# Optimization experiments

Hardware: AMD Instinct MI355X
Metric: run time of the kernel (lower is better)

Reference implementation:

```python
import jax, jax.numpy as jnp
import numpy as np

B, S, D = 2, 4096, 512
H = 8
W = 512            # local attention window size
HD = D // H        # head dim
NC = S // W        # number of chunks
HALF = W // 2      # symmetric half-window


def setup_inputs() -> dict:
    key = jax.random.key(0)
    ks = jax.random.split(key, 12)
    s = 1.0 / np.sqrt(D)
    return {
        "val": jax.random.normal(ks[0], (B, S, D), jnp.float32),
        "Wq": jax.random.normal(ks[1], (D, D), jnp.float32) * s,
        "bq": jnp.zeros((D,), jnp.float32),
        "Wk": jax.random.normal(ks[2], (D, D), jnp.float32) * s,
        "bk": jnp.zeros((D,), jnp.float32),
        "Wv": jax.random.normal(ks[3], (D, D), jnp.float32) * s,
        "bv": jnp.zeros((D,), jnp.float32),
        "Wo": jax.random.normal(ks[4], (D, D), jnp.float32) * s,
        "bo": jnp.zeros((D,), jnp.float32),
        "gamma": jnp.ones((D,), jnp.float32),
        "beta": jnp.zeros((D,), jnp.float32),
    }


def _heads(x):
    # [B,S,D] -> [B,H,S,HD]
    return x.reshape(B, S, H, HD).transpose(0, 2, 1, 3)


def _gather_neighbors(x):
    # x: [B,H,S,HD] -> [B,H,NC,3W,HD] (prev | cur | next chunk, zero-padded at ends)
    xp = jnp.pad(x, ((0, 0), (0, 0), (W, W), (0, 0)))
    xc = xp.reshape(B, H, NC + 2, W, HD)
    return jnp.concatenate([xc[:, :, :-2], xc[:, :, 1:-1], xc[:, :, 2:]], axis=3)


def _local_attention(x, Wq, bq, Wk, bk, Wv, bv, Wo, bo):
    q = _heads(x @ Wq + bq)
    k = _heads(x @ Wk + bk)
    v = _heads(x @ Wv + bv)

    qc = q.reshape(B, H, NC, W, HD)            # chunked queries
    kn = _gather_neighbors(k)                  # [B,H,NC,3W,HD]
    vn = _gather_neighbors(v)

    scale = 1.0 / np.sqrt(HD)
    scores = jnp.einsum("bhcqd,bhckd->bhcqk", qc, kn) * scale  # [B,H,NC,W,3W]

    # banded mask: key relative position in [-HALF, HALF], and key index in [0,S)
    qi = jnp.arange(W)[:, None]
    kj = jnp.arange(3 * W)[None, :]
    band = jnp.abs(kj - W - qi) <= HALF                          # [W,3W]
    key_pos = (jnp.arange(NC)[:, None, None] - 1) * W + kj[None]  # [NC,1,3W]
    valid = (key_pos >= 0) & (key_pos < S)                       # [NC,1,3W]
    mask = band[None] & valid                                    # [NC,W,3W]

    scores = jnp.where(mask[None, None], scores, jnp.float32(-1e9))
    p = jax.nn.softmax(scores, axis=-1)
    o = jnp.einsum("bhcqk,bhckd->bhcqd", p, vn)                  # [B,H,NC,W,HD]
    o = o.reshape(B, H, S, HD).transpose(0, 2, 1, 3).reshape(B, S, D)
    return o @ Wo + bo


def _layer_norm(x, gamma, beta, eps=1e-5):
    mu = jnp.mean(x, axis=-1, keepdims=True)
    var = jnp.mean(jnp.square(x - mu), axis=-1, keepdims=True)
    return (x - mu) * jax.lax.rsqrt(var + eps) * gamma + beta


def reference(val, Wq, bq, Wk, bk, Wv, bv, Wo, bo, gamma, beta):
    attn_out = _local_attention(val, Wq, bq, Wk, bk, Wv, bv, Wo, bo)
    return _layer_norm(val + attn_out, gamma, beta)
```

## Files before the change

kernel.cpp:

```cpp
#include <hip/hip_runtime.h>
#include <hip/hip_bf16.h>

#define BATCH 2
#define SEQ   4096
#define DIM   512
#define NHEAD 8
#define HDIM  64
#define ROWS  (BATCH*SEQ)

typedef float  fx4   __attribute__((ext_vector_type(4)));
typedef __bf16 bf16x8 __attribute__((ext_vector_type(8)));
typedef unsigned short ushort_t;
typedef unsigned short usx4 __attribute__((ext_vector_type(4)));
typedef unsigned short usx8 __attribute__((ext_vector_type(8)));

static __device__ __forceinline__ float b2f(ushort_t v) {
    union { unsigned int u; float f; } c; c.u = ((unsigned int)v) << 16; return c.f;
}
static __device__ __forceinline__ ushort_t f2b(float f) {
    union { float f; unsigned int u; } c; c.f = f;
    unsigned int u = c.u;
    unsigned int r = (u + 0x7FFFu + ((u >> 16) & 1u)) >> 16;
    return (ushort_t)r;
}
static __device__ __forceinline__ void gload16(const ushort_t* g, ushort_t* l) {
    __builtin_amdgcn_global_load_lds(
        (const __attribute__((address_space(1))) unsigned int*)g,
        (__attribute__((address_space(3))) unsigned int*)l, 16, 0, 0);
}

__global__ __launch_bounds__(256) void cvt_bf16_kernel(const float* __restrict__ x,
                                                       ushort_t* __restrict__ y, int n) {
    int i = (blockIdx.x * 256 + threadIdx.x) * 4;
    if (i < n) {
        fx4 v = *(const fx4*)(x + i);
        usx4 o; o.x = f2b(v.x); o.y = f2b(v.y); o.z = f2b(v.z); o.w = f2b(v.w);
        *(usx4*)(y + i) = o;
    }
}

__global__ __launch_bounds__(256) void transpose4_bf16_kernel(
    const float* __restrict__ W0, const float* __restrict__ W1,
    const float* __restrict__ W2, const float* __restrict__ W3,
    ushort_t* __restrict__ T0, ushort_t* __restrict__ T1,
    ushort_t* __restrict__ T2, ushort_t* __restrict__ T3) {
    const float* W; ushort_t* WT;
    switch (blockIdx.y) {
        case 0: W = W0; WT = T0; break;
        case 1: W = W1; WT = T1; break;
        case 2: W = W2; WT = T2; break;
        default: W = W3; WT = T3; break;
    }
    __shared__ float tile[64][65];
    int r0 = (blockIdx.x & 7) * 64;
    int c0 = (blockIdx.x >> 3) * 64;
    int tid = threadIdx.x;
    for (int idx = tid; idx < 4096; idx += 256) {
        int rr = idx >> 6, cc = idx & 63;
        tile[rr][cc] = W[(c0 + rr) * 512 + (r0 + cc)];
    }
    __syncthreads();
    for (int idx = tid; idx < 4096; idx += 256) {
        int rr = idx >> 6, cc = idx & 63;
        WT[(size_t)(r0 + rr) * 512 + (c0 + cc)] = f2b(tile[cc][rr]);
    }
}

__global__ __launch_bounds__(256) void gemm128_kernel(
    const ushort_t* __restrict__ A,
    const ushort_t* __restrict__ BT0, const ushort_t* __restrict__ BT1, const ushort_t* __restrict__ BT2,
    const float* __restrict__ b0, const float* __restrict__ b1, const float* __restrict__ b2,
    ushort_t* __restrict__ C0, ushort_t* __restrict__ C1, ushort_t* __restrict__ C2) {

    const ushort_t* BT; const float* bias; ushort_t* C;
    if (blockIdx.z == 0)      { BT = BT0; bias = b0; C = C0; }
    else if (blockIdx.z == 1) { BT = BT1; bias = b1; C = C1; }
    else                      { BT = BT2; bias = b2; C = C2; }

    __shared__ ushort_t As[128 * 32];
    __shared__ ushort_t Bs[128 * 32];

    const int tid  = threadIdx.x;
    const int wave = tid >> 6;
    const int lane = tid & 63;
    const int lm   = lane & 15;
    const int quad = lane >> 4;
    const int wm   = wave >> 1;
    const int wn   = wave & 1;

    const int m0t = blockIdx.x * 128;
    const int n0t = blockIdx.y * 128;

    const int srow = tid >> 2, sgc = tid & 3;
    const ushort_t* ga0 = A  + (size_t)(m0t + srow) * 512 + sgc * 8;
    const ushort_t* ga1 = A  + (size_t)(m0t + srow + 64) * 512 + sgc * 8;
    const ushort_t* gb0 = BT + (size_t)(n0t + srow) * 512 + sgc * 8;
    const ushort_t* gb1 = BT + (size_t)(n0t + srow + 64) * 512 + sgc * 8;
    ushort_t* la0 = As + tid * 8;
    ushort_t* la1 = As + (tid + 256) * 8;
    ushort_t* lb0 = Bs + tid * 8;
    ushort_t* lb1 = Bs + (tid + 256) * 8;

    const int aoff = (wm * 64 + lm) * 32 + quad * 8;
    const int boff = (wn * 64 + lm) * 32 + quad * 8;

    fx4 acc[4][4];
    #pragma unroll
    for (int i = 0; i < 4; ++i)
        #pragma unroll
        for (int j = 0; j < 4; ++j) acc[i][j] = 0;

    for (int k0 = 0; k0 < 512; k0 += 32) {
        __syncthreads();
        gload16(ga0 + k0, la0);
        gload16(ga1 + k0, la1);
        gload16(gb0 + k0, lb0);
        gload16(gb1 + k0, lb1);
        __syncthreads();

        bf16x8 af[4], bfr[4];
        #pragma unroll
        for (int ms = 0; ms < 4; ++ms) af[ms]  = *(const bf16x8*)&As[aoff + ms * 512];
        #pragma unroll
        for (int ns = 0; ns < 4; ++ns) bfr[ns] = *(const bf16x8*)&Bs[boff + ns * 512];
        #pragma unroll
        for (int ms = 0; ms < 4; ++ms)
            #pragma unroll
            for (int ns = 0; ns < 4; ++ns)
                acc[ms][ns] = __builtin_amdgcn_mfma_f32_16x16x32_bf16(af[ms], bfr[ns], acc[ms][ns], 0, 0, 0);
    }

    const int crow0 = m0t + wm * 64 + quad * 4;
    const int ccol0 = n0t + wn * 64 + lm;

    if (blockIdx.z == 2) {
        #pragma unroll
        for (int ns = 0; ns < 4; ++ns) {
            int col = ccol0 + ns * 16;
            int h = col >> 6, d = col & 63;
            float bv = bias[col];
            #pragma unroll
            for (int ms = 0; ms < 4; ++ms) {
                int m = crow0 + ms * 16;
                int bb = m >> 12, s0 = m & 4095;
                usx4 o;
                o.x = f2b(acc[ms][ns][0] + bv); o.y = f2b(acc[ms][ns][1] + bv);
                o.z = f2b(acc[ms][ns][2] + bv); o.w = f2b(acc[ms][ns][3] + bv);
                *(usx4*)(C + (((size_t)(bb * 8 + h) * 64 + d) * 4096 + s0)) = o;
            }
        }
    } else {
        #pragma unroll
        for (int ns = 0; ns < 4; ++ns) {
            int col = ccol0 + ns * 16;
            float bv = bias[col];
            #pragma unroll
            for (int ms = 0; ms < 4; ++ms) {
                #pragma unroll
                for (int r = 0; r < 4; ++r) {
                    C[(size_t)(crow0 + ms * 16 + r) * 512 + col] = f2b(acc[ms][ns][r] + bv);
                }
            }
        }
    }
}

__global__ __launch_bounds__(256) void attn_mfma_kernel(
    const ushort_t* __restrict__ Qb, const ushort_t* __restrict__ Kb,
    const ushort_t* __restrict__ Vt, ushort_t* __restrict__ Ob) {

    __shared__ ushort_t Klds[64 * 64];
    __shared__ ushort_t Vlds[64 * 64];
    __shared__ ushort_t Plds[4 * 16 * 64];

    const int tid  = threadIdx.x;
    const int wave = tid >> 6;
    const int lane = tid & 63;
    const int lm   = lane & 15;
    const int quad = lane >> 4;

    const int bh = blockIdx.y;
    const int b = bh >> 3, h = bh & 7;
    const int q0 = blockIdx.x * 64;
    const int qw = q0 + wave * 16;

    const ushort_t* qp = Qb + ((size_t)(b * SEQ + qw + lm)) * 512 + h * 64 + quad * 8;
    bf16x8 qf0 = *(const bf16x8*)qp;
    bf16x8 qf1 = *(const bf16x8*)(qp + 32);

    int koff[2][4], voff[2][4];
    #pragma unroll
    for (int ks = 0; ks < 2; ++ks) {
        #pragma unroll
        for (int tn = 0; tn < 4; ++tn) {
            int key = tn * 16 + lm;
            koff[ks][tn] = key * 64 + (((ks * 4 + quad) ^ (key & 7)) * 8);
            int d = tn * 16 + lm;
            voff[ks][tn] = d * 64 + (((ks * 4 + quad) ^ (d & 7)) * 8);
        }
    }
    int poff[2];
    #pragma unroll
    for (int ks = 0; ks < 2; ++ks)
        poff[ks] = lm * 64 + (((ks * 4 + quad) ^ (lm & 7) ^ ((lm >> 3) << 1)) * 8);
    int pwoff[4][4];
    #pragma unroll
    for (int tn = 0; tn < 4; ++tn) {
        #pragma unroll
        for (int r = 0; r < 4; ++r) {
            int row = quad * 4 + r;
            int col = tn * 16 + lm;
            pwoff[tn][r] = row * 64 + (((col >> 3) ^ (row & 7) ^ ((row >> 3) << 1)) * 8) + (col & 7);
        }
    }
    ushort_t* Pl = Plds + wave * 1024;

    const int skey = tid >> 3;
    const int sdg  = tid & 7;
    const size_t kgbase = ((size_t)b * SEQ) * 512 + h * 64 + sdg * 8;
    const size_t vgbase = ((size_t)bh * 64) * 4096 + sdg * 8;
    const int l0 = skey * 64 + ((sdg ^ (skey & 7)) * 8);
    const int l1 = l0 + 32 * 64;

    fx4 oacc[4];
    oacc[0] = 0; oacc[1] = 0; oacc[2] = 0; oacc[3] = 0;
    float l[4] = {0.f, 0.f, 0.f, 0.f};

    for (int kt = 0; kt < 9; ++kt) {
        int ts = q0 - 256 + kt * 64;
        if (ts < 0 || ts >= SEQ) continue;

        __syncthreads();
        {
            usx8 k0v = *(const usx8*)(Kb + kgbase + (size_t)(ts + skey) * 512);
            usx8 k1v = *(const usx8*)(Kb + kgbase + (size_t)(ts + skey + 32) * 512);
            usx8 v0v = *(const usx8*)(Vt + vgbase + (size_t)skey * 4096 + ts);
            usx8 v1v = *(const usx8*)(Vt + vgbase + (size_t)(skey + 32) * 4096 + ts);
            *(usx8*)&Klds[l0] = k0v;
            *(usx8*)&Klds[l1] = k1v;
            *(usx8*)&Vlds[l0] = v0v;
            *(usx8*)&Vlds[l1] = v1v;
        }
        __syncthreads();

        fx4 sacc[4];
        sacc[0] = 0; sacc[1] = 0; sacc[2] = 0; sacc[3] = 0;
        #pragma unroll
        for (int ks = 0; ks < 2; ++ks) {
            bf16x8 a = ks ? qf1 : qf0;
            #pragma unroll
            for (int tn = 0; tn < 4; ++tn) {
                bf16x8 bk = *(const bf16x8*)&Klds[koff[ks][tn]];
                sacc[tn] = __builtin_amdgcn_mfma_f32_16x16x32_bf16(a, bk, sacc[tn], 0, 0, 0);
            }
        }

        float ps[4] = {0.f, 0.f, 0.f, 0.f};
        #pragma unroll
        for (int tn = 0; tn < 4; ++tn) {
            int kg = ts + tn * 16 + lm;
            #pragma unroll
            for (int r = 0; r < 4; ++r) {
                int qg = qw + quad * 4 + r;
                int dlt = kg - qg;
                float p = (dlt <= 256 && dlt >= -256) ? __expf(sacc[tn][r] * 0.125f) : 0.0f;
                ps[r] += p;
                Pl[pwoff[tn][r]] = f2b(p);
            }
        }
        #pragma unroll
        for (int r = 0; r < 4; ++r) {
            float v = ps[r];
            v += __shfl_xor(v, 1); v += __shfl_xor(v, 2);
            v += __shfl_xor(v, 4); v += __shfl_xor(v, 8);
            l[r] += v;
        }

        #pragma unroll
        for (int ks = 0; ks < 2; ++ks) {
            bf16x8 ap = *(const bf16x8*)&Pl[poff[ks]];
            #pragma unroll
            for (int tn = 0; tn < 4; ++tn) {
                bf16x8 bv = *(const bf16x8*)&Vlds[voff[ks][tn]];
                oacc[tn] = __builtin_amdgcn_mfma_f32_16x16x32_bf16(ap, bv, oacc[tn], 0, 0, 0);
            }
        }
    }

    #pragma unroll
    for (int r = 0; r < 4; ++r) l[r] = 1.0f / l[r];
    ushort_t* ob = Ob + ((size_t)(b * SEQ + qw + quad * 4)) * 512 + h * 64 + lm;
    #pragma unroll
    for (int tn = 0; tn < 4; ++tn) {
        #pragma unroll
        for (int r = 0; r < 4; ++r) {
            ob[(size_t)r * 512 + tn * 16] = f2b(oacc[tn][r] * l[r]);
        }
    }
}

__global__ __launch_bounds__(256) void ln_kernel(
    const float* __restrict__ x, const ushort_t* __restrict__ ob,
    const float* __restrict__ gamma, const float* __restrict__ beta,
    float* __restrict__ out) {

    int row  = blockIdx.x * 4 + (threadIdx.x >> 6);
    int lane = threadIdx.x & 63;

    const float*    xp = x  + (size_t)row * 512 + lane * 8;
    const ushort_t* op = ob + (size_t)row * 512 + lane * 8;

    fx4 xa = ((const fx4*)xp)[0];
    fx4 xb = ((const fx4*)xp)[1];
    usx4 oa = ((const usx4*)op)[0];
    usx4 oc = ((const usx4*)op)[1];
    fx4 va, vb;
    va.x = xa.x + b2f(oa.x); va.y = xa.y + b2f(oa.y); va.z = xa.z + b2f(oa.z); va.w = xa.w + b2f(oa.w);
    vb.x = xb.x + b2f(oc.x); vb.y = xb.y + b2f(oc.y); vb.z = xb.z + b2f(oc.z); vb.w = xb.w + b2f(oc.w);

    float s = va.x + va.y + va.z + va.w + vb.x + vb.y + vb.z + vb.w;
    #pragma unroll
    for (int m = 32; m > 0; m >>= 1) s += __shfl_xor(s, m);
    float mu = s * (1.0f / 512.0f);

    fx4 da = va - mu;
    fx4 db = vb - mu;
    float ss = da.x*da.x + da.y*da.y + da.z*da.z + da.w*da.w
             + db.x*db.x + db.y*db.y + db.z*db.z + db.w*db.w;
    #pragma unroll
    for (int m = 32; m > 0; m >>= 1) ss += __shfl_xor(ss, m);
    float rstd = rsqrtf(ss * (1.0f / 512.0f) + 1e-5f);

    const fx4* gp = (const fx4*)(gamma + lane * 8);
    const fx4* bp = (const fx4*)(beta  + lane * 8);
    fx4 g0 = gp[0], g1 = gp[1], b0 = bp[0], b1 = bp[1];

    float* outp = out + (size_t)row * 512 + lane * 8;
    fx4 r0 = da * rstd * g0 + b0;
    fx4 r1 = db * rstd * g1 + b1;
    ((fx4*)outp)[0] = r0;
    ((fx4*)outp)[1] = r1;
}

extern "C" void kernel_launch(void* const* d_in, const int* in_sizes, int n_in,
                              void* d_out, int out_size, void* d_ws, size_t ws_size,
                              hipStream_t stream) {
    const float* val   = (const float*)d_in[0];
    const float* Wq    = (const float*)d_in[1];
    const float* bq    = (const float*)d_in[2];
    const float* Wk    = (const float*)d_in[3];
    const float* bk    = (const float*)d_in[4];
    const float* Wv    = (const float*)d_in[5];
    const float* bv    = (const float*)d_in[6];
    const float* Wo    = (const float*)d_in[7];
    const float* bo    = (const float*)d_in[8];
    const float* gamma = (const float*)d_in[9];
    const float* beta  = (const float*)d_in[10];
    float* out = (float*)d_out;

    char* w = (char*)d_ws;
    ushort_t* xb    = (ushort_t*)w; w += (size_t)ROWS * 512 * 2;
    ushort_t* WqT   = (ushort_t*)w; w += 512 * 512 * 2;
    ushort_t* WkT   = (ushort_t*)w; w += 512 * 512 * 2;
    ushort_t* WvT   = (ushort_t*)w; w += 512 * 512 * 2;
    ushort_t* WoT   = (ushort_t*)w; w += 512 * 512 * 2;
    ushort_t* Qb    = (ushort_t*)w; w += (size_t)ROWS * 512 * 2;
    ushort_t* Kb    = (ushort_t*)w; w += (size_t)ROWS * 512 * 2;
    ushort_t* Vtb   = (ushort_t*)w; w += (size_t)ROWS * 512 * 2;
    ushort_t* attnb = (ushort_t*)w; w += (size_t)ROWS * 512 * 2;
    ushort_t* obuf  = (ushort_t*)w; w += (size_t)ROWS * 512 * 2;

    int nelem = ROWS * 512;
    cvt_bf16_kernel<<<nelem / (256 * 4), 256, 0, stream>>>(val, xb, nelem);
    transpose4_bf16_kernel<<<dim3(64, 4), 256, 0, stream>>>(
        Wq, Wk, Wv, Wo, WqT, WkT, WvT, WoT);

    gemm128_kernel<<<dim3(ROWS / 128, 4, 3), 256, 0, stream>>>(
        xb, WqT, WkT, WvT, bq, bk, bv, Qb, Kb, Vtb);

    attn_mfma_kernel<<<dim3(SEQ / 64, BATCH * NHEAD), 256, 0, stream>>>(Qb, Kb, Vtb, attnb);

    gemm128_kernel<<<dim3(ROWS / 128, 4, 1), 256, 0, stream>>>(
        attnb, WoT, WoT, WoT, bo, bo, bo, obuf, obuf, obuf);

    ln_kernel<<<ROWS / 4, 256, 0, stream>>>(val, obuf, gamma, beta, out);
}
```

Measured before the change: 169.6 us.

## Enlarge attention query tile, prefetch K/V, skip masked tiles, MFMA row sums

The attention kernel now gives each block 128 queries (32 per wave), so every K/V tile loaded into LDS is reused by twice as many queries. The next K/V tile is prefetched into registers while the current one is computed. Waves skip tiles that lie entirely outside their band, and the mask check runs only on edge tiles. Row sums of P come from an extra MFMA against a ones vector instead of shuffle reductions. The GEMM also stages a 64-wide K slice per barrier pair, halving the number of barriers. In exchange the kernel uses more registers and launches half as many attention blocks, which could reduce occupancy.

```diff
diff --git a/kernel.cpp b/kernel.cpp
--- a/kernel.cpp
+++ b/kernel.cpp
@@ -77,8 +77,8 @@
     else if (blockIdx.z == 1) { BT = BT1; bias = b1; C = C1; }
     else                      { BT = BT2; bias = b2; C = C2; }
 
-    __shared__ ushort_t As[128 * 32];
-    __shared__ ushort_t Bs[128 * 32];
+    __shared__ ushort_t As[2][128 * 32];
+    __shared__ ushort_t Bs[2][128 * 32];
 
     const int tid  = threadIdx.x;
     const int wave = tid >> 6;
@@ -96,10 +96,6 @@
     const ushort_t* ga1 = A  + (size_t)(m0t + srow + 64) * 512 + sgc * 8;
     const ushort_t* gb0 = BT + (size_t)(n0t + srow) * 512 + sgc * 8;
     const ushort_t* gb1 = BT + (size_t)(n0t + srow + 64) * 512 + sgc * 8;
-    ushort_t* la0 = As + tid * 8;
-    ushort_t* la1 = As + (tid + 256) * 8;
-    ushort_t* lb0 = Bs + tid * 8;
-    ushort_t* lb1 = Bs + (tid + 256) * 8;
 
     const int aoff = (wm * 64 + lm) * 32 + quad * 8;
     const int boff = (wn * 64 + lm) * 32 + quad * 8;
@@ -110,24 +106,30 @@
         #pragma unroll
         for (int j = 0; j < 4; ++j) acc[i][j] = 0;
 
-    for (int k0 = 0; k0 < 512; k0 += 32) {
+    for (int k0 = 0; k0 < 512; k0 += 64) {
         __syncthreads();
-        gload16(ga0 + k0, la0);
-        gload16(ga1 + k0, la1);
-        gload16(gb0 + k0, lb0);
-        gload16(gb1 + k0, lb1);
+        #pragma unroll
+        for (int p = 0; p < 2; ++p) {
+            gload16(ga0 + k0 + p * 32, &As[p][tid * 8]);
+            gload16(ga1 + k0 + p * 32, &As[p][(tid + 256) * 8]);
+            gload16(gb0 + k0 + p * 32, &Bs[p][tid * 8]);
+            gload16(gb1 + k0 + p * 32, &Bs[p][(tid + 256) * 8]);
+        }
         __syncthreads();
 
-        bf16x8 af[4], bfr[4];
-        #pragma unroll
-        for (int ms = 0; ms < 4; ++ms) af[ms]  = *(const bf16x8*)&As[aoff + ms * 512];
-        #pragma unroll
-        for (int ns = 0; ns < 4; ++ns) bfr[ns] = *(const bf16x8*)&Bs[boff + ns * 512];
-        #pragma unroll
-        for (int ms = 0; ms < 4; ++ms)
-            #pragma unroll
-            for (int ns = 0; ns < 4; ++ns)
-                acc[ms][ns] = __builtin_amdgcn_mfma_f32_16x16x32_bf16(af[ms], bfr[ns], acc[ms][ns], 0, 0, 0);
+        #pragma unroll
+        for (int p = 0; p < 2; ++p) {
+            bf16x8 af[4], bfr[4];
+            #pragma unroll
+            for (int ms = 0; ms < 4; ++ms) af[ms]  = *(const bf16x8*)&As[p][aoff + ms * 512];
+            #pragma unroll
+            for (int ns = 0; ns < 4; ++ns) bfr[ns] = *(const bf16x8*)&Bs[p][boff + ns * 512];
+            #pragma unroll
+            for (int ms = 0; ms < 4; ++ms)
+                #pragma unroll
+                for (int ns = 0; ns < 4; ++ns)
+                    acc[ms][ns] = __builtin_amdgcn_mfma_f32_16x16x32_bf16(af[ms], bfr[ns], acc[ms][ns], 0, 0, 0);
+        }
     }
 
     const int crow0 = m0t + wm * 64 + quad * 4;
@@ -171,7 +173,7 @@
 
     __shared__ ushort_t Klds[64 * 64];
     __shared__ ushort_t Vlds[64 * 64];
-    __shared__ ushort_t Plds[4 * 16 * 64];
+    __shared__ ushort_t Plds[4 * 32 * 72];
 
     const int tid  = threadIdx.x;
     const int wave = tid >> 6;
@@ -181,12 +183,16 @@
 
     const int bh = blockIdx.y;
     const int b = bh >> 3, h = bh & 7;
-    const int q0 = blockIdx.x * 64;
-    const int qw = q0 + wave * 16;
-
-    const ushort_t* qp = Qb + ((size_t)(b * SEQ + qw + lm)) * 512 + h * 64 + quad * 8;
-    bf16x8 qf0 = *(const bf16x8*)qp;
-    bf16x8 qf1 = *(const bf16x8*)(qp + 32);
+    const int q0 = blockIdx.x * 128;
+    const int qw = q0 + wave * 32;
+
+    bf16x8 qf[2][2];
+    #pragma unroll
+    for (int qs = 0; qs < 2; ++qs) {
+        const ushort_t* qp = Qb + ((size_t)(b * SEQ + qw + qs * 16 + lm)) * 512 + h * 64 + quad * 8;
+        qf[qs][0] = *(const bf16x8*)qp;
+        qf[qs][1] = *(const bf16x8*)(qp + 32);
+    }
 
     int koff[2][4], voff[2][4];
     #pragma unroll
@@ -199,21 +205,13 @@
             voff[ks][tn] = d * 64 + (((ks * 4 + quad) ^ (d & 7)) * 8);
         }
     }
-    int poff[2];
-    #pragma unroll
-    for (int ks = 0; ks < 2; ++ks)
-        poff[ks] = lm * 64 + (((ks * 4 + quad) ^ (lm & 7) ^ ((lm >> 3) << 1)) * 8);
-    int pwoff[4][4];
-    #pragma unroll
-    for (int tn = 0; tn < 4; ++tn) {
-        #pragma unroll
-        for (int r = 0; r < 4; ++r) {
-            int row = quad * 4 + r;
-            int col = tn * 16 + lm;
-            pwoff[tn][r] = row * 64 + (((col >> 3) ^ (row & 7) ^ ((row >> 3) << 1)) * 8) + (col & 7);
-        }
-    }
-    ushort_t* Pl = Plds + wave * 1024;
+    ushort_t* Pw = Plds + wave * (32 * 72);
+    int pread[2][2];
+    #pragma unroll
+    for (int qs = 0; qs < 2; ++qs)
+        #pragma unroll
+        for (int ks = 0; ks < 2; ++ks)
+            pread[qs][ks] = (qs * 16 + lm) * 72 + ks * 32 + quad * 8;
 
     const int skey = tid >> 3;
     const int sdg  = tid & 7;
@@ -222,80 +220,124 @@
     const int l0 = skey * 64 + ((sdg ^ (skey & 7)) * 8);
     const int l1 = l0 + 32 * 64;
 
-    fx4 oacc[4];
-    oacc[0] = 0; oacc[1] = 0; oacc[2] = 0; oacc[3] = 0;
-    float l[4] = {0.f, 0.f, 0.f, 0.f};
-
-    for (int kt = 0; kt < 9; ++kt) {
-        int ts = q0 - 256 + kt * 64;
-        if (ts < 0 || ts >= SEQ) continue;
-
+    const int klo = (q0 >= 256) ? 0 : ((256 - q0) >> 6);
+    const int khi = min(9, (4288 - q0) >> 6);
+    const int wlo = wave >> 1, whi = 8 + (wave >> 1);
+    const int flo = 1 + (wave >> 1), fhi = 7 + (wave >> 1);
+
+    bf16x8 onesf;
+    {
+        __bf16 o = (lm == 0) ? (__bf16)1.0f : (__bf16)0.0f;
+        #pragma unroll
+        for (int j = 0; j < 8; ++j) onesf[j] = o;
+    }
+
+    fx4 oacc[2][4];
+    #pragma unroll
+    for (int qs = 0; qs < 2; ++qs)
+        #pragma unroll
+        for (int tn = 0; tn < 4; ++tn) oacc[qs][tn] = 0;
+    fx4 lacc[2];
+    lacc[0] = 0; lacc[1] = 0;
+
+    usx8 kn0, kn1, vn0, vn1;
+    {
+        int ts = q0 - 256 + klo * 64;
+        kn0 = *(const usx8*)(Kb + kgbase + (size_t)(ts + skey) * 512);
+        kn1 = *(const usx8*)(Kb + kgbase + (size_t)(ts + skey + 32) * 512);
+        vn0 = *(const usx8*)(Vt + vgbase + (size_t)skey * 4096 + ts);
+        vn1 = *(const usx8*)(Vt + vgbase + (size_t)(skey + 32) * 4096 + ts);
+    }
+
+    for (int kt = klo; kt <= khi; ++kt) {
+        const int ts = q0 - 256 + kt * 64;
         __syncthreads();
-        {
-            usx8 k0v = *(const usx8*)(Kb + kgbase + (size_t)(ts + skey) * 512);
-            usx8 k1v = *(const usx8*)(Kb + kgbase + (size_t)(ts + skey + 32) * 512);
-            usx8 v0v = *(const usx8*)(Vt + vgbase + (size_t)skey * 4096 + ts);
-            usx8 v1v = *(const usx8*)(Vt + vgbase + (size_t)(skey + 32) * 4096 + ts);
-            *(usx8*)&Klds[l0] = k0v;
-            *(usx8*)&Klds[l1] = k1v;
-            *(usx8*)&Vlds[l0] = v0v;
-            *(usx8*)&Vlds[l1] = v1v;
-        }
+        *(usx8*)&Klds[l0] = kn0;
+        *(usx8*)&Klds[l1] = kn1;
+        *(usx8*)&Vlds[l0] = vn0;
+        *(usx8*)&Vlds[l1] = vn1;
         __syncthreads();
 
-        fx4 sacc[4];
-        sacc[0] = 0; sacc[1] = 0; sacc[2] = 0; sacc[3] = 0;
-        #pragma unroll
-        for (int ks = 0; ks < 2; ++ks) {
-            bf16x8 a = ks ? qf1 : qf0;
+        if (kt < khi) {
+            int t2 = ts + 64;
+            kn0 = *(const usx8*)(Kb + kgbase + (size_t)(t2 + skey) * 512);
+            kn1 = *(const usx8*)(Kb + kgbase + (size_t)(t2 + skey + 32) * 512);
+            vn0 = *(const usx8*)(Vt + vgbase + (size_t)skey * 4096 + t2);
+            vn1 = *(const usx8*)(Vt + vgbase + (size_t)(skey + 32) * 4096 + t2);
+        }
+
+        if (kt < wlo || kt > whi) continue;
+
+        bf16x8 kf[2][4];
+        #pragma unroll
+        for (int ks = 0; ks < 2; ++ks)
+            #pragma unroll
+            for (int tn = 0; tn < 4; ++tn)
+                kf[ks][tn] = *(const bf16x8*)&Klds[koff[ks][tn]];
+        fx4 sacc[2][4];
+        #pragma unroll
+        for (int qs = 0; qs < 2; ++qs)
+            #pragma unroll
+            for (int tn = 0; tn < 4; ++tn) sacc[qs][tn] = 0;
+        #pragma unroll
+        for (int ks = 0; ks < 2; ++ks)
             #pragma unroll
             for (int tn = 0; tn < 4; ++tn) {
-                bf16x8 bk = *(const bf16x8*)&Klds[koff[ks][tn]];
-                sacc[tn] = __builtin_amdgcn_mfma_f32_16x16x32_bf16(a, bk, sacc[tn], 0, 0, 0);
+                sacc[0][tn] = __builtin_amdgcn_mfma_f32_16x16x32_bf16(qf[0][ks], kf[ks][tn], sacc[0][tn], 0, 0, 0);
+                sacc[1][tn] = __builtin_amdgcn_mfma_f32_16x16x32_bf16(qf[1][ks], kf[ks][tn], sacc[1][tn], 0, 0, 0);
             }
-        }
-
-        float ps[4] = {0.f, 0.f, 0.f, 0.f};
-        #pragma unroll
-        for (int tn = 0; tn < 4; ++tn) {
-            int kg = ts + tn * 16 + lm;
-            #pragma unroll
-            for (int r = 0; r < 4; ++r) {
-                int qg = qw + quad * 4 + r;
-                int dlt = kg - qg;
-                float p = (dlt <= 256 && dlt >= -256) ? __expf(sacc[tn][r] * 0.125f) : 0.0f;
-                ps[r] += p;
-                Pl[pwoff[tn][r]] = f2b(p);
+
+        const bool edge = (kt < flo) || (kt > fhi);
+        #pragma unroll
+        for (int qs = 0; qs < 2; ++qs) {
+            #pragma unroll
+            for (int tn = 0; tn < 4; ++tn) {
+                int kg = ts + tn * 16 + lm;
+                #pragma unroll
+                for (int r = 0; r < 4; ++r) {
+                    float p = __expf(sacc[qs][tn][r] * 0.125f);
+                    if (edge) {
+                        int dlt = kg - (qw + qs * 16 + quad * 4 + r);
+                        p = (dlt <= 256 && dlt >= -256) ? p : 0.0f;
+                    }
+                    Pw[(qs * 16 + quad * 4 + r) * 72 + tn * 16 + lm] = f2b(p);
+                }
             }
         }
+
+        bf16x8 vf[2][4];
+        #pragma unroll
+        for (int ks = 0; ks < 2; ++ks)
+            #pragma unroll
+            for (int tn = 0; tn < 4; ++tn)
+                vf[ks][tn] = *(const bf16x8*)&Vlds[voff[ks][tn]];
+        #pragma unroll
+        for (int qs = 0; qs < 2; ++qs) {
+            #pragma unroll
+            for (int ks = 0; ks < 2; ++ks) {
+                bf16x8 ap = *(const bf16x8*)&Pw[pread[qs][ks]];
+                lacc[qs] = __builtin_amdgcn_mfma_f32_16x16x32_bf16(ap, onesf, lacc[qs], 0, 0, 0);
+                #pragma unroll
+                for (int tn = 0; tn < 4; ++tn)
+                    oacc[qs][tn] = __builtin_amdgcn_mfma_f32_16x16x32_bf16(ap, vf[ks][tn], oacc[qs][tn], 0, 0, 0);
+            }
+        }
+    }
+
+    #pragma unroll
+    for (int qs = 0; qs < 2; ++qs) {
+        float linv[4];
         #pragma unroll
         for (int r = 0; r < 4; ++r) {
-            float v = ps[r];
-            v += __shfl_xor(v, 1); v += __shfl_xor(v, 2);
-            v += __shfl_xor(v, 4); v += __shfl_xor(v, 8);
-            l[r] += v;
-        }
-
-        #pragma unroll
-        for (int ks = 0; ks < 2; ++ks) {
-            bf16x8 ap = *(const bf16x8*)&Pl[poff[ks]];
-            #pragma unroll
-            for (int tn = 0; tn < 4; ++tn) {
-                bf16x8 bv = *(const bf16x8*)&Vlds[voff[ks][tn]];
-                oacc[tn] = __builtin_amdgcn_mfma_f32_16x16x32_bf16(ap, bv, oacc[tn], 0, 0, 0);
-            }
-        }
-    }
-
-    #pragma unroll
-    for (int r = 0; r < 4; ++r) l[r] = 1.0f / l[r];
-    ushort_t* ob = Ob + ((size_t)(b * SEQ + qw + quad * 4)) * 512 + h * 64 + lm;
-    #pragma unroll
-    for (int tn = 0; tn < 4; ++tn) {
-        #pragma unroll
-        for (int r = 0; r < 4; ++r) {
-            ob[(size_t)r * 512 + tn * 16] = f2b(oacc[tn][r] * l[r]);
-        }
+            float lv = __shfl(lacc[qs][r], (lane & 48));
+            linv[r] = 1.0f / lv;
+        }
+        ushort_t* ob = Ob + ((size_t)(b * SEQ + qw + qs * 16 + quad * 4)) * 512 + h * 64 + lm;
+        #pragma unroll
+        for (int tn = 0; tn < 4; ++tn)
+            #pragma unroll
+            for (int r = 0; r < 4; ++r)
+                ob[(size_t)r * 512 + tn * 16] = f2b(oacc[qs][tn][r] * linv[r]);
     }
 }
 
@@ -378,7 +420,7 @@
     gemm128_kernel<<<dim3(ROWS / 128, 4, 3), 256, 0, stream>>>(
         xb, WqT, WkT, WvT, bq, bk, bv, Qb, Kb, Vtb);
 
-    attn_mfma_kernel<<<dim3(SEQ / 64, BATCH * NHEAD), 256, 0, stream>>>(Qb, Kb, Vtb, attnb);
+    attn_mfma_kernel<<<dim3(SEQ / 128, BATCH * NHEAD), 256, 0, stream>>>(Qb, Kb, Vtb, attnb);
 
     gemm128_kernel<<<dim3(ROWS / 128, 4, 1), 256, 0, stream>>>(
         attnb, WoT, WoT, WoT, bo, bo, bo, obuf, obuf, obuf);
```

Result: no change. 172.7 us (+1.9%).
